# Performance work log

Measured on AMD Instinct MI355X. Metric: run time of the kernel, lower is better.

Reference implementation:

```python
import jax, jax.numpy as jnp
import numpy as np

B, N, D_FEAT = 16, 1024, 64
NPOINT, RADIUS, NSAMPLE = 512, 0.2, 32
EPS = 1e-5


def _square_distance(src, dst):
    # src [b,S,3], dst [b,N,3] -> [b,S,N]
    d = -2.0 * jnp.einsum('bsc,bnc->bsn', src, dst)
    d = d + jnp.sum(src * src, -1)[:, :, None]
    d = d + jnp.sum(dst * dst, -1)[:, None, :]
    return d


def _fps(xyz, npoint):
    # xyz [b,N,3] -> indices [b,npoint]; seeded by point farthest from the mean
    b, n, _ = xyz.shape
    centroid = jnp.mean(xyz, axis=1, keepdims=True)
    distance = jnp.minimum(jnp.full((b, n), 1e10, xyz.dtype),
                           jnp.sum((xyz - centroid) ** 2, -1))
    farthest = jnp.argmax(distance, -1)
    bidx = jnp.arange(b)

    def body(carry, _):
        dist, far = carry
        c = xyz[bidx[:, None], far[:, None]]  # [b,1,3]
        dist = jnp.minimum(dist, jnp.sum((xyz - c) ** 2, -1))
        return (dist, jnp.argmax(dist, -1)), far

    _, idx = jax.lax.scan(body, (distance, farthest), None, length=npoint)
    return idx.T  # [b, npoint]


def _gather(points, idx):
    # points [b,N,C], idx [b,...] -> [b,...,C]
    return jax.vmap(lambda p, i: p[i])(points, idx)


def _query_ball(radius, nsample, xyz, new_xyz):
    # faithful to torch: mask out-of-radius with N, full sort, take first nsample,
    # replace sentinels by the first (closest-index) in-ball point
    b, n, _ = xyz.shape
    sqr = _square_distance(new_xyz, xyz)  # [b,S,N]
    idx = jnp.where(sqr > radius ** 2, n, jnp.arange(n)[None, None, :])
    idx = jnp.sort(idx, axis=-1)[:, :, :nsample]
    first = idx[:, :, :1]
    return jnp.where(idx == n, first, idx)


def _qbn(x):
    # QBN_RM training mode: divide by per-channel RMS of detached activations
    mean = jnp.mean(jax.lax.stop_gradient(x) ** 2, axis=(0, 2, 3))
    return x / jnp.sqrt(mean + EPS)[None, :, None, None]


def _qrelu(x):
    # scale each 3-vector by mod / max(mod, 1), coefficient detached
    b3, c, s, k = x.shape
    b = b3 // 3
    xd = jax.lax.stop_gradient(x).reshape(b, 3, c, s, k)
    mod = jnp.sqrt(jnp.sum(xd * xd, axis=1))  # [b,c,s,k]
    coeff = mod / jnp.maximum(mod, 1.0)
    return jnp.broadcast_to(coeff[:, None], (b, 3, c, s, k)).reshape(b3, c, s, k) * x


def _qmaxpool(x):
    # our_mpool1d with kernel (1, nsample): pick the max-modulus sample over K,
    # gather the same index for all 3 quaternion components
    b3, c, s, k = x.shape
    b = b3 // 3
    x5 = x.reshape(b, 3, c, s, k)
    mod = jnp.sum(jax.lax.stop_gradient(x5) ** 2, axis=1)  # argmax of mod == argmax of mod^2
    idx = jnp.argmax(mod, axis=-1)  # [b,c,s]
    idxb = jnp.broadcast_to(idx[:, None, :, :, None], (b, 3, c, s, 1))
    y = jnp.take_along_axis(x5, idxb, axis=-1)[..., 0]  # [b,3,c,s]
    return y.reshape(b3, c, s)


def setup_inputs() -> dict:
    key = jax.random.key(0)
    k1, k2, k3, k4, k5 = jax.random.split(key, 5)
    xyz = jax.random.normal(k1, (B, 3, N), dtype=jnp.float32)
    points = jax.random.normal(k2, (B * 3, D_FEAT, N), dtype=jnp.float32)
    W0 = jax.random.normal(k3, (64, 66), dtype=jnp.float32) * np.sqrt(2.0 / 66)
    W1 = jax.random.normal(k4, (64, 64), dtype=jnp.float32) * np.sqrt(2.0 / 64)
    W2 = jax.random.normal(k5, (128, 64), dtype=jnp.float32) * np.sqrt(2.0 / 64)
    return {"xyz": xyz, "points": points, "W0": W0, "W1": W1, "W2": W2}


def reference(xyz, points, W0, W1, W2):
    xyz_t = xyz.transpose(0, 2, 1)      # [B,N,3]
    pts_t = points.transpose(0, 2, 1)   # [B*3,N,D]

    fps_idx = _fps(xyz_t, NPOINT)                       # [B,S]
    new_xyz = _gather(xyz_t, fps_idx)                   # [B,S,3]
    idx = _query_ball(RADIUS, NSAMPLE, xyz_t, new_xyz)  # [B,S,K]

    g_xyz = _gather(xyz_t, idx)                         # [B,S,K,3]
    g_norm = g_xyz - new_xyz[:, :, None, :]
    gx = g_xyz.transpose(0, 3, 1, 2).reshape(B * 3, NPOINT, NSAMPLE, 1)
    gn = g_norm.transpose(0, 3, 1, 2).reshape(B * 3, NPOINT, NSAMPLE, 1)
    idx3 = jnp.broadcast_to(idx[:, None], (B, 3, NPOINT, NSAMPLE)).reshape(B * 3, NPOINT, NSAMPLE)
    gp = _gather(pts_t, idx3)                           # [B*3,S,K,D]

    x = jnp.concatenate([gn, gx, gp], axis=-1)          # [B*3,S,K,D+2]
    x = x.transpose(0, 3, 1, 2)                         # [B*3,D+2,S,K]
    for W in (W0, W1, W2):
        x = jnp.einsum('bcsk,oc->bosk', x, W)           # 1x1 conv, no bias
        x = _qrelu(_qbn(x))
    new_feat = _qmaxpool(x)                             # [B*3,128,S]
    return new_xyz.transpose(0, 2, 1), new_feat
```

## Files before the change

kernel.cpp:

```cpp
#include <hip/hip_runtime.h>

typedef unsigned int u32;

#define NB 16
#define NPT 1024
#define NP 512
#define NS 32
#define DF 64
#define RAD2 0.04f
#define EPSQ 1e-5f
#define CNTF 786432.0f
#define NGRP 8192
#define TCAP 96
#define TSLOT 128
#define NTILE_MAX 2731

__device__ __forceinline__ float rmul(float a, float b){ return __fmul_rn(a,b); }
__device__ __forceinline__ float radd(float a, float b){ return __fadd_rn(a,b); }
__device__ __forceinline__ float sq3(float a, float b, float c){
  return radd(radd(rmul(a,a), rmul(b,b)), rmul(c,c));
}

__device__ __forceinline__ float wave_sum64(float v){
  #pragma unroll
  for(int m=1;m<64;m<<=1) v += __shfl_xor(v, m, 64);
  return v;
}

template<int PT>
__global__ __launch_bounds__(256) void fps_combo(const float* __restrict__ xyz,
                                                 float* __restrict__ out0,
                                                 const float* __restrict__ pts,
                                                 float* __restrict__ ptsT,
                                                 u32* __restrict__ witem){
  const int bid = blockIdx.x;
  const int t = threadIdx.x;
  if(bid >= NB){
    const int gid = (bid - NB)*256 + t;
    if(gid < NTILE_MAX*TSLOT) witem[gid] = 0xFFFFFFFFu;
    if constexpr(PT){
      const int w = gid >> 6, ln = gid & 63;
      if(w < 48*16){
        const int b3 = w >> 4, n0 = (w & 15) << 6;
        const float* src = pts + (((size_t)b3*64 + ln) << 10);
        float* dst = ptsT + (((size_t)b3*1024 + n0) << 6) + ln;
        #pragma unroll 4
        for(int i=0;i<64;i++) dst[(size_t)i << 6] = src[n0 + i];
      }
    }
    return;
  }
  if(t >= 64) return;
  const int lane = t;
  const int b = bid;
  const float* xb = xyz + b*3*NPT;
  float px[16], py[16], pz[16], dist[16];
  #pragma unroll
  for(int j=0;j<16;j++){
    const int n = lane*16 + j;
    px[j] = xb[n]; py[j] = xb[NPT+n]; pz[j] = xb[2*NPT+n];
  }
  float sx=0.f, sy=0.f, sz=0.f;
  #pragma unroll
  for(int j=0;j<16;j++){ sx+=px[j]; sy+=py[j]; sz+=pz[j]; }
  sx = wave_sum64(sx); sy = wave_sum64(sy); sz = wave_sum64(sz);
  const float cx = sx/1024.f, cy = sy/1024.f, cz = sz/1024.f;
  float m = -1.f; int mi = 0;
  #pragma unroll
  for(int j=0;j<16;j++){
    float dx = px[j]-cx, dy = py[j]-cy, dz = pz[j]-cz;
    float d = fminf(1e10f, sq3(dx,dy,dz));
    dist[j] = d;
    if(d > m){ m = d; mi = lane*16 + j; }
  }
  #pragma unroll
  for(int msk=1; msk<64; msk<<=1){
    float ov = __shfl_xor(m, msk, 64); int oi = __shfl_xor(mi, msk, 64);
    if(ov > m || (ov == m && oi < mi)){ m = ov; mi = oi; }
  }
  int far = mi;
  for(int it=0; it<NP; ++it){
    const float qx = xb[far], qy = xb[NPT+far], qz = xb[2*NPT+far];
    if(lane == 0){
      out0[(b*3+0)*NP + it] = qx;
      out0[(b*3+1)*NP + it] = qy;
      out0[(b*3+2)*NP + it] = qz;
    }
    m = -1.f; mi = 0;
    #pragma unroll
    for(int j=0;j<16;j++){
      float dx = px[j]-qx, dy = py[j]-qy, dz = pz[j]-qz;
      float nd = sq3(dx,dy,dz);
      float d = fminf(dist[j], nd);
      dist[j] = d;
      if(d > m){ m = d; mi = lane*16 + j; }
    }
    #pragma unroll
    for(int msk=1; msk<64; msk<<=1){
      float ov = __shfl_xor(m, msk, 64); int oi = __shfl_xor(mi, msk, 64);
      if(ov > m || (ov == m && oi < mi)){ m = ov; mi = oi; }
    }
    far = mi;
  }
}

__global__ __launch_bounds__(256) void ball_kernel(const float* __restrict__ xyz,
                                                   const float* __restrict__ out0,
                                                   int* __restrict__ idxb,
                                                   int* __restrict__ cntb){
  const int gw = (blockIdx.x * 256 + threadIdx.x) >> 6;
  const int lane = threadIdx.x & 63;
  const int b = gw >> 9;
  const int s = gw & 511;
  const float s0 = out0[(b*3+0)*NP + s];
  const float s1 = out0[(b*3+1)*NP + s];
  const float s2 = out0[(b*3+2)*NP + s];
  const float ss = sq3(s0,s1,s2);
  const float* xb = xyz + b*3*NPT;
  int base = 0;
  int* row = idxb + (b*NP + s)*NS;
  for(int chk=0; chk<16 && base<NS; ++chk){
    const int n = chk*64 + lane;
    float d0 = xb[n], d1 = xb[NPT+n], d2 = xb[2*NPT+n];
    float dd = sq3(d0,d1,d2);
    float p  = radd(radd(rmul(s0,d0), rmul(s1,d1)), rmul(s2,d2));
    float sqr = radd(radd(rmul(-2.0f,p), ss), dd);
    bool inc = !(sqr > RAD2);
    unsigned long long mask = __ballot(inc);
    if(inc){
      int slot = base + __popcll(mask & ((1ull<<lane)-1ull));
      if(slot < NS) row[slot] = n;
    }
    base += __popcll(mask);
  }
  if(lane==0) cntb[gw] = (base < NS) ? base : NS;
}

__global__ __launch_bounds__(256) void pack_kernel(const int* __restrict__ cntb,
                                                   const int* __restrict__ idxb,
                                                   u32* __restrict__ witem,
                                                   int* __restrict__ ntile_dev){
  __shared__ int tsum[256];
  const int t = threadIdx.x;
  int s0 = 0;
  #pragma unroll 4
  for(int i=0;i<32;i++) s0 += cntb[t*32+i];
  tsum[t] = s0;
  __syncthreads();
  for(int ofs=1; ofs<256; ofs<<=1){
    int v = (t >= ofs) ? tsum[t-ofs] : 0;
    __syncthreads();
    tsum[t] += v;
    __syncthreads();
  }
  int m = tsum[t] - s0;
  if(t==255) *ntile_dev = (tsum[255] + TCAP - 1) / TCAP;
  for(int i=0;i<32;i++){
    int g = t*32+i; int c = cntb[g];
    int tile = m / TCAP; int slot = m - TCAP*tile;
    const int* row = idxb + g*NS;
    for(int j=0;j<c;j++){
      witem[tile*TSLOT + slot + j] = (u32)((g<<15) | (j<<10) | row[j]);
    }
    m += c;
  }
}

template<int DEPTH, int PT>
__global__ __launch_bounds__(384) void pass_kernel(
  const float* __restrict__ xyz, const float* __restrict__ ptsrc,
  const float* __restrict__ W0, const float* __restrict__ W1, const float* __restrict__ W2,
  const float* __restrict__ out0, const u32* __restrict__ witem,
  const int* __restrict__ cntb, const int* __restrict__ ntile_dev,
  const float* __restrict__ inv1, const float* __restrict__ inv2,
  float* __restrict__ part, float* __restrict__ out1)
{
  const int t = threadIdx.x;
  const int c3 = t >> 7;
  const int r  = t & 127;
  const int lane = t & 63;
  const int wv = t >> 6;
  const int bi = blockIdx.x;
  constexpr int nch = (DEPTH==3) ? 128 : 64;

  if(bi >= *ntile_dev){
    if(t < nch) part[bi*nch + t] = 0.f;
    return;
  }

  __shared__ float sq[3][128][17];
  __shared__ float wstat[6][128];
  for(int i=t; i<6*128; i+=384) (&wstat[0][0])[i] = 0.f;
  __syncthreads();

  const u32 w = witem[bi*TSLOT + r];
  const bool valid = (w != 0xFFFFFFFFu);
  const int bs = valid ? (int)(w >> 15) : 0;
  const int j  = valid ? (int)((w >> 10) & 31) : 1;
  const int n  = valid ? (int)(w & 1023) : 0;
  const int b = bs >> 9;
  const int s = bs & 511;
  const int b3 = b*3 + c3;
  const int cv = cntb[bs];
  const float wgt = valid ? ((j==0) ? (float)(33 - cv) : 1.0f) : 0.0f;

  const float gx = xyz[b3*NPT + n];
  const float cx = out0[b3*NP + s];
  float x0[66];
  x0[0] = gx - cx;
  x0[1] = gx;
  if constexpr(PT){
    const float4* pr4 = reinterpret_cast<const float4*>(ptsrc + (((size_t)b3<<10) + (size_t)n)*DF);
    #pragma unroll
    for(int q=0;q<16;q++){
      float4 v = pr4[q];
      x0[2+4*q] = v.x; x0[3+4*q] = v.y; x0[4+4*q] = v.z; x0[5+4*q] = v.w;
    }
  } else {
    const float* pr = ptsrc + ((size_t)b3*DF)*NPT + n;
    #pragma unroll
    for(int c=0;c<DF;c++) x0[2+c] = pr[(size_t)c*NPT];
  }

  float y1[64];
  #pragma unroll
  for(int ch=0; ch<4; ++ch){
    float acc[16];
    #pragma unroll
    for(int oo=0;oo<16;oo++){
      const int o = ch*16+oo;
      float a = 0.f;
      #pragma unroll
      for(int c=0;c<66;c++) a = fmaf(W0[o*66+c], x0[c], a);
      acc[oo] = a;
    }
    if constexpr(DEPTH == 1){
      #pragma unroll
      for(int oo=0;oo<16;oo++){
        float v = wave_sum64(acc[oo]*acc[oo]*wgt);
        if(lane==0) wstat[wv][ch*16+oo] += v;
      }
    } else {
      #pragma unroll
      for(int oo=0;oo<16;oo++){
        const int o = ch*16+oo;
        float xp = acc[oo] * inv1[o];
        acc[oo] = xp;
        sq[c3][r][oo] = xp*xp;
      }
      __syncthreads();
      #pragma unroll
      for(int oo=0;oo<16;oo++){
        float m2 = (sq[0][r][oo] + sq[1][r][oo]) + sq[2][r][oo];
        float mod = sqrtf(m2);
        float cf = (mod >= 1.f) ? 1.f : mod;
        y1[ch*16+oo] = cf * acc[oo];
      }
      __syncthreads();
    }
  }
  if constexpr(DEPTH == 1){
    __syncthreads();
    if(t < 64){
      float sv = 0.f;
      #pragma unroll
      for(int wq=0;wq<6;wq++) sv += wstat[wq][t];
      part[bi*64 + t] = sv;
    }
    return;
  }

  float y2[64];
  #pragma unroll
  for(int ch=0; ch<4; ++ch){
    float acc[16];
    #pragma unroll
    for(int oo=0;oo<16;oo++){
      const int o = ch*16+oo;
      float a = 0.f;
      #pragma unroll
      for(int c=0;c<64;c++) a = fmaf(W1[o*64+c], y1[c], a);
      acc[oo] = a;
    }
    if constexpr(DEPTH == 2){
      #pragma unroll
      for(int oo=0;oo<16;oo++){
        float v = wave_sum64(acc[oo]*acc[oo]*wgt);
        if(lane==0) wstat[wv][ch*16+oo] += v;
      }
    } else {
      #pragma unroll
      for(int oo=0;oo<16;oo++){
        const int o = ch*16+oo;
        float xp = acc[oo] * inv2[o];
        acc[oo] = xp;
        sq[c3][r][oo] = xp*xp;
      }
      __syncthreads();
      #pragma unroll
      for(int oo=0;oo<16;oo++){
        float m2 = (sq[0][r][oo] + sq[1][r][oo]) + sq[2][r][oo];
        float mod = sqrtf(m2);
        float cf = (mod >= 1.f) ? 1.f : mod;
        y2[ch*16+oo] = cf * acc[oo];
      }
      __syncthreads();
    }
  }
  if constexpr(DEPTH == 2){
    __syncthreads();
    if(t < 64){
      float sv = 0.f;
      #pragma unroll
      for(int wq=0;wq<6;wq++) sv += wstat[wq][t];
      part[bi*64 + t] = sv;
    }
    return;
  }

  #pragma unroll
  for(int ch=0; ch<8; ++ch){
    float a3[16];
    #pragma unroll
    for(int oo=0;oo<16;oo++){
      const int o = ch*16+oo;
      float a = 0.f;
      #pragma unroll
      for(int c=0;c<64;c++) a = fmaf(W2[o*64+c], y2[c], a);
      a3[oo] = a;
      sq[c3][r][oo] = a;
    }
    __syncthreads();
    if(c3 == 0){
      #pragma unroll
      for(int oo=0;oo<16;oo++){
        float a0 = sq[0][r][oo], a1 = sq[1][r][oo], a2 = sq[2][r][oo];
        float m2 = radd(radd(rmul(a0,a0), rmul(a1,a1)), rmul(a2,a2));
        float v = wave_sum64(m2*wgt);
        if(lane==0) wstat[wv][ch*16+oo] += v;
        if(valid && j==0){
          float bvv = m2; int bjj = 0;
          for(int jj=1; jj<cv; ++jj){
            float c0 = sq[0][r+jj][oo], c1 = sq[1][r+jj][oo], c2 = sq[2][r+jj][oo];
            float mm = radd(radd(rmul(c0,c0), rmul(c1,c1)), rmul(c2,c2));
            if(mm > bvv){ bvv = mm; bjj = jj; }
          }
          const int o = ch*16+oo;
          #pragma unroll
          for(int cc=0;cc<3;cc++){
            out1[(((size_t)(3*b+cc))*128 + o)*NP + s] = sq[cc][r+bjj][oo];
          }
        }
      }
    }
    __syncthreads();
  }
  if(t < 128){
    part[bi*128 + t] = wstat[0][t] + wstat[1][t];
  }
}

__global__ __launch_bounds__(256) void fin_kernel(const float* __restrict__ part, int nblk, int nch,
                                                  float* __restrict__ inv){
  const int o = blockIdx.x;
  const int t = threadIdx.x;
  float sum = 0.f;
  for(int i=t; i<nblk; i+=256) sum += part[(size_t)i*nch + o];
  sum = wave_sum64(sum);
  __shared__ float red[4];
  if((t&63)==0) red[t>>6] = sum;
  __syncthreads();
  if(t==0){
    float tot = (red[0]+red[1])+(red[2]+red[3]);
    inv[o] = 1.0f / sqrtf(tot/CNTF + EPSQ);
  }
}

__global__ __launch_bounds__(256) void scale_kernel(float* __restrict__ out,
                                                    const float* __restrict__ inv3){
  const int tid = blockIdx.x*256 + threadIdx.x;
  if(tid >= NB*128*NP) return;
  const int s = tid & 511;
  const int o = (tid >> 9) & 127;
  const int b = tid >> 16;
  float* base = out + NB*3*NP;
  const size_t str = (size_t)128*NP;
  size_t i0 = ((size_t)(b*3)*128 + o)*NP + s;
  float iv = inv3[o];
  float a0 = base[i0] * iv;
  float a1 = base[i0+str] * iv;
  float a2 = base[i0+2*str] * iv;
  float m2 = (a0*a0 + a1*a1) + a2*a2;
  float mod = sqrtf(m2);
  float cf = (mod >= 1.f) ? 1.f : mod;
  base[i0] = cf*a0; base[i0+str] = cf*a1; base[i0+2*str] = cf*a2;
}

extern "C" void kernel_launch(void* const* d_in, const int* in_sizes, int n_in,
                              void* d_out, int out_size, void* d_ws, size_t ws_size,
                              hipStream_t stream){
  const float* xyz = (const float*)d_in[0];
  const float* pts = (const float*)d_in[1];
  const float* W0  = (const float*)d_in[2];
  const float* W1  = (const float*)d_in[3];
  const float* W2  = (const float*)d_in[4];
  float* out = (float*)d_out;

  char* p = (char*)d_ws;
  auto carve = [&](size_t bytes)->char*{
    char* q = p; p += (bytes + 255) & ~(size_t)255; return q;
  };
  int*   idxb      = (int*)  carve((size_t)NGRP*NS*4);
  int*   cntb      = (int*)  carve((size_t)NGRP*4);
  u32*   witem     = (u32*)  carve((size_t)NTILE_MAX*TSLOT*4);
  int*   ntile_dev = (int*)  carve(256);
  float* part1     = (float*)carve((size_t)NTILE_MAX*64*4);
  float* part2     = (float*)carve((size_t)NTILE_MAX*64*4);
  float* part3     = (float*)carve((size_t)NTILE_MAX*128*4);
  float* inv1      = (float*)carve(64*4);
  float* inv2      = (float*)carve(64*4);
  float* inv3      = (float*)carve(128*4);
  size_t base_need = (size_t)(p - (char*)d_ws);
  float* ptsT      = (float*)p;
  const size_t pt_bytes = (size_t)48*1024*64*4;
  const bool use_pt = (ws_size >= base_need + pt_bytes);

  float* out1 = out + NB*3*NP;

  const int copyblk = (NTILE_MAX*TSLOT + 255)/256;
  if(use_pt) fps_combo<1><<<NB + copyblk, 256, 0, stream>>>(xyz, out, pts, ptsT, witem);
  else       fps_combo<0><<<NB + copyblk, 256, 0, stream>>>(xyz, out, pts, nullptr, witem);

  ball_kernel<<<2048, 256, 0, stream>>>(xyz, out, idxb, cntb);
  pack_kernel<<<1, 256, 0, stream>>>(cntb, idxb, witem, ntile_dev);

  if(use_pt){
    pass_kernel<1,1><<<NTILE_MAX, 384, 0, stream>>>(xyz, ptsT, W0, W1, W2, out, witem, cntb, ntile_dev, nullptr, nullptr, part1, nullptr);
    fin_kernel<<<64, 256, 0, stream>>>(part1, NTILE_MAX, 64, inv1);
    pass_kernel<2,1><<<NTILE_MAX, 384, 0, stream>>>(xyz, ptsT, W0, W1, W2, out, witem, cntb, ntile_dev, inv1, nullptr, part2, nullptr);
    fin_kernel<<<64, 256, 0, stream>>>(part2, NTILE_MAX, 64, inv2);
    pass_kernel<3,1><<<NTILE_MAX, 384, 0, stream>>>(xyz, ptsT, W0, W1, W2, out, witem, cntb, ntile_dev, inv1, inv2, part3, out1);
  } else {
    pass_kernel<1,0><<<NTILE_MAX, 384, 0, stream>>>(xyz, pts, W0, W1, W2, out, witem, cntb, ntile_dev, nullptr, nullptr, part1, nullptr);
    fin_kernel<<<64, 256, 0, stream>>>(part1, NTILE_MAX, 64, inv1);
    pass_kernel<2,0><<<NTILE_MAX, 384, 0, stream>>>(xyz, pts, W0, W1, W2, out, witem, cntb, ntile_dev, inv1, nullptr, part2, nullptr);
    fin_kernel<<<64, 256, 0, stream>>>(part2, NTILE_MAX, 64, inv2);
    pass_kernel<3,0><<<NTILE_MAX, 384, 0, stream>>>(xyz, pts, W0, W1, W2, out, witem, cntb, ntile_dev, inv1, inv2, part3, out1);
  }
  fin_kernel<<<128, 256, 0, stream>>>(part3, NTILE_MAX, 128, inv3);
  scale_kernel<<<(NB*128*NP + 255)/256, 256, 0, stream>>>(out, inv3);
}
```

Before: 925.7 us.

## Use DPP tree argmax in FPS, parallel scan pack, fuse final stats with scale

```diff
diff --git a/kernel.cpp b/kernel.cpp
--- a/kernel.cpp
+++ b/kernel.cpp
@@ -25,6 +25,44 @@
   #pragma unroll
   for(int m=1;m<64;m<<=1) v += __shfl_xor(v, m, 64);
   return v;
+}
+
+#define DPPCOMB(CTRL) do{ \
+  float _ov = __int_as_float(__builtin_amdgcn_mov_dpp(__float_as_int(m), (CTRL), 0xF, 0xF, true)); \
+  int   _oi = __builtin_amdgcn_mov_dpp(mi, (CTRL), 0xF, 0xF, true); \
+  if(_ov > m || (_ov == m && _oi < mi)){ m = _ov; mi = _oi; } \
+}while(0)
+
+__device__ __forceinline__ int wave_argmax1024(const float* dist, int lane){
+  float v8[8]; int j8[8];
+  #pragma unroll
+  for(int q=0;q<8;q++){
+    float l = dist[q], r = dist[q+8];
+    bool tk = (r > l);
+    v8[q] = tk ? r : l; j8[q] = tk ? q+8 : q;
+  }
+  float v4[4]; int j4[4];
+  #pragma unroll
+  for(int q=0;q<4;q++){
+    bool tk = (v8[q+4] > v8[q]);
+    v4[q] = tk ? v8[q+4] : v8[q]; j4[q] = tk ? j8[q+4] : j8[q];
+  }
+  float v2[2]; int j2[2];
+  #pragma unroll
+  for(int q=0;q<2;q++){
+    bool tk = (v4[q+2] > v4[q]);
+    v2[q] = tk ? v4[q+2] : v4[q]; j2[q] = tk ? j4[q+2] : j4[q];
+  }
+  bool tk = (v2[1] > v2[0]);
+  float m = tk ? v2[1] : v2[0];
+  int mi = lane*16 + (tk ? j2[1] : j2[0]);
+  DPPCOMB(0xB1);
+  DPPCOMB(0x4E);
+  DPPCOMB(0x124);
+  DPPCOMB(0x128);
+  DPPCOMB(0x142);
+  DPPCOMB(0x143);
+  return __builtin_amdgcn_readlane(mi, 63);
 }
 
 template<int PT>
@@ -65,20 +103,12 @@
   for(int j=0;j<16;j++){ sx+=px[j]; sy+=py[j]; sz+=pz[j]; }
   sx = wave_sum64(sx); sy = wave_sum64(sy); sz = wave_sum64(sz);
   const float cx = sx/1024.f, cy = sy/1024.f, cz = sz/1024.f;
-  float m = -1.f; int mi = 0;
   #pragma unroll
   for(int j=0;j<16;j++){
     float dx = px[j]-cx, dy = py[j]-cy, dz = pz[j]-cz;
-    float d = fminf(1e10f, sq3(dx,dy,dz));
-    dist[j] = d;
-    if(d > m){ m = d; mi = lane*16 + j; }
-  }
-  #pragma unroll
-  for(int msk=1; msk<64; msk<<=1){
-    float ov = __shfl_xor(m, msk, 64); int oi = __shfl_xor(mi, msk, 64);
-    if(ov > m || (ov == m && oi < mi)){ m = ov; mi = oi; }
-  }
-  int far = mi;
+    dist[j] = fminf(1e10f, sq3(dx,dy,dz));
+  }
+  int far = wave_argmax1024(dist, lane);
   for(int it=0; it<NP; ++it){
     const float qx = xb[far], qy = xb[NPT+far], qz = xb[2*NPT+far];
     if(lane == 0){
@@ -86,21 +116,13 @@
       out0[(b*3+1)*NP + it] = qy;
       out0[(b*3+2)*NP + it] = qz;
     }
-    m = -1.f; mi = 0;
     #pragma unroll
     for(int j=0;j<16;j++){
       float dx = px[j]-qx, dy = py[j]-qy, dz = pz[j]-qz;
       float nd = sq3(dx,dy,dz);
-      float d = fminf(dist[j], nd);
-      dist[j] = d;
-      if(d > m){ m = d; mi = lane*16 + j; }
-    }
-    #pragma unroll
-    for(int msk=1; msk<64; msk<<=1){
-      float ov = __shfl_xor(m, msk, 64); int oi = __shfl_xor(mi, msk, 64);
-      if(ov > m || (ov == m && oi < mi)){ m = ov; mi = oi; }
-    }
-    far = mi;
+      dist[j] = fminf(dist[j], nd);
+    }
+    far = wave_argmax1024(dist, lane);
   }
 }
 
@@ -136,33 +158,39 @@
   if(lane==0) cntb[gw] = (base < NS) ? base : NS;
 }
 
-__global__ __launch_bounds__(256) void pack_kernel(const int* __restrict__ cntb,
-                                                   const int* __restrict__ idxb,
-                                                   u32* __restrict__ witem,
-                                                   int* __restrict__ ntile_dev){
-  __shared__ int tsum[256];
+__global__ __launch_bounds__(1024) void pack_kernel(const int* __restrict__ cntb,
+                                                    const int* __restrict__ idxb,
+                                                    u32* __restrict__ witem,
+                                                    int* __restrict__ ntile_dev){
   const int t = threadIdx.x;
-  int s0 = 0;
-  #pragma unroll 4
-  for(int i=0;i<32;i++) s0 += cntb[t*32+i];
-  tsum[t] = s0;
+  const int lane = t & 63;
+  const int wv = t >> 6;
+  int c[8]; int s0 = 0;
+  #pragma unroll
+  for(int i=0;i<8;i++){ c[i] = cntb[t*8+i]; s0 += c[i]; }
+  int pre = s0;
+  #pragma unroll
+  for(int d=1; d<64; d<<=1){
+    int v = __shfl_up(pre, d, 64);
+    if(lane >= d) pre += v;
+  }
+  __shared__ int wsum[16];
+  if(lane==63) wsum[wv] = pre;
   __syncthreads();
-  for(int ofs=1; ofs<256; ofs<<=1){
-    int v = (t >= ofs) ? tsum[t-ofs] : 0;
-    __syncthreads();
-    tsum[t] += v;
-    __syncthreads();
-  }
-  int m = tsum[t] - s0;
-  if(t==255) *ntile_dev = (tsum[255] + TCAP - 1) / TCAP;
-  for(int i=0;i<32;i++){
-    int g = t*32+i; int c = cntb[g];
-    int tile = m / TCAP; int slot = m - TCAP*tile;
+  int wo = 0;
+  #pragma unroll
+  for(int w=0;w<16;w++) if(w < wv) wo += wsum[w];
+  int m = wo + pre - s0;
+  if(t==1023) *ntile_dev = (wo + pre + TCAP - 1) / TCAP;
+  #pragma unroll
+  for(int i=0;i<8;i++){
+    const int g = t*8+i; const int cc = c[i];
+    const int tile = m / TCAP; const int slot = m - TCAP*tile;
     const int* row = idxb + g*NS;
-    for(int j=0;j<c;j++){
+    for(int j=0;j<cc;j++){
       witem[tile*TSLOT + slot + j] = (u32)((g<<15) | (j<<10) | row[j]);
     }
-    m += c;
+    m += cc;
   }
 }
 
@@ -181,12 +209,8 @@
   const int lane = t & 63;
   const int wv = t >> 6;
   const int bi = blockIdx.x;
-  constexpr int nch = (DEPTH==3) ? 128 : 64;
-
-  if(bi >= *ntile_dev){
-    if(t < nch) part[bi*nch + t] = 0.f;
-    return;
-  }
+
+  if(bi >= *ntile_dev) return;
 
   __shared__ float sq[3][128][17];
   __shared__ float wstat[6][128];
@@ -360,10 +384,12 @@
   }
 }
 
-__global__ __launch_bounds__(256) void fin_kernel(const float* __restrict__ part, int nblk, int nch,
+__global__ __launch_bounds__(256) void fin_kernel(const float* __restrict__ part,
+                                                  const int* __restrict__ ntile_dev, int nch,
                                                   float* __restrict__ inv){
   const int o = blockIdx.x;
   const int t = threadIdx.x;
+  const int nblk = *ntile_dev;
   float sum = 0.f;
   for(int i=t; i<nblk; i+=256) sum += part[(size_t)i*nch + o];
   sum = wave_sum64(sum);
@@ -376,24 +402,38 @@
   }
 }
 
-__global__ __launch_bounds__(256) void scale_kernel(float* __restrict__ out,
-                                                    const float* __restrict__ inv3){
-  const int tid = blockIdx.x*256 + threadIdx.x;
-  if(tid >= NB*128*NP) return;
-  const int s = tid & 511;
-  const int o = (tid >> 9) & 127;
-  const int b = tid >> 16;
+__global__ __launch_bounds__(256) void fin3_scale(const float* __restrict__ part3,
+                                                  const int* __restrict__ ntile_dev,
+                                                  float* __restrict__ out){
+  const int o = blockIdx.x;
+  const int t = threadIdx.x;
+  const int nblk = *ntile_dev;
+  float sum = 0.f;
+  for(int i=t; i<nblk; i+=256) sum += part3[(size_t)i*128 + o];
+  sum = wave_sum64(sum);
+  __shared__ float red[4];
+  __shared__ float sinv;
+  if((t&63)==0) red[t>>6] = sum;
+  __syncthreads();
+  if(t==0){
+    float tot = (red[0]+red[1])+(red[2]+red[3]);
+    sinv = 1.0f / sqrtf(tot/CNTF + EPSQ);
+  }
+  __syncthreads();
+  const float iv = sinv;
   float* base = out + NB*3*NP;
   const size_t str = (size_t)128*NP;
-  size_t i0 = ((size_t)(b*3)*128 + o)*NP + s;
-  float iv = inv3[o];
-  float a0 = base[i0] * iv;
-  float a1 = base[i0+str] * iv;
-  float a2 = base[i0+2*str] * iv;
-  float m2 = (a0*a0 + a1*a1) + a2*a2;
-  float mod = sqrtf(m2);
-  float cf = (mod >= 1.f) ? 1.f : mod;
-  base[i0] = cf*a0; base[i0+str] = cf*a1; base[i0+2*str] = cf*a2;
+  for(int idx=t; idx<NB*NP; idx+=256){
+    const int b = idx >> 9, s = idx & 511;
+    size_t i0 = ((size_t)(b*3)*128 + o)*NP + s;
+    float a0 = base[i0] * iv;
+    float a1 = base[i0+str] * iv;
+    float a2 = base[i0+2*str] * iv;
+    float m2 = (a0*a0 + a1*a1) + a2*a2;
+    float mod = sqrtf(m2);
+    float cf = (mod >= 1.f) ? 1.f : mod;
+    base[i0] = cf*a0; base[i0+str] = cf*a1; base[i0+2*str] = cf*a2;
+  }
 }
 
 extern "C" void kernel_launch(void* const* d_in, const int* in_sizes, int n_in,
@@ -432,21 +472,20 @@
   else       fps_combo<0><<<NB + copyblk, 256, 0, stream>>>(xyz, out, pts, nullptr, witem);
 
   ball_kernel<<<2048, 256, 0, stream>>>(xyz, out, idxb, cntb);
-  pack_kernel<<<1, 256, 0, stream>>>(cntb, idxb, witem, ntile_dev);
+  pack_kernel<<<1, 1024, 0, stream>>>(cntb, idxb, witem, ntile_dev);
 
   if(use_pt){
     pass_kernel<1,1><<<NTILE_MAX, 384, 0, stream>>>(xyz, ptsT, W0, W1, W2, out, witem, cntb, ntile_dev, nullptr, nullptr, part1, nullptr);
-    fin_kernel<<<64, 256, 0, stream>>>(part1, NTILE_MAX, 64, inv1);
+    fin_kernel<<<64, 256, 0, stream>>>(part1, ntile_dev, 64, inv1);
     pass_kernel<2,1><<<NTILE_MAX, 384, 0, stream>>>(xyz, ptsT, W0, W1, W2, out, witem, cntb, ntile_dev, inv1, nullptr, part2, nullptr);
-    fin_kernel<<<64, 256, 0, stream>>>(part2, NTILE_MAX, 64, inv2);
+    fin_kernel<<<64, 256, 0, stream>>>(part2, ntile_dev, 64, inv2);
     pass_kernel<3,1><<<NTILE_MAX, 384, 0, stream>>>(xyz, ptsT, W0, W1, W2, out, witem, cntb, ntile_dev, inv1, inv2, part3, out1);
   } else {
     pass_kernel<1,0><<<NTILE_MAX, 384, 0, stream>>>(xyz, pts, W0, W1, W2, out, witem, cntb, ntile_dev, nullptr, nullptr, part1, nullptr);
-    fin_kernel<<<64, 256, 0, stream>>>(part1, NTILE_MAX, 64, inv1);
+    fin_kernel<<<64, 256, 0, stream>>>(part1, ntile_dev, 64, inv1);
     pass_kernel<2,0><<<NTILE_MAX, 384, 0, stream>>>(xyz, pts, W0, W1, W2, out, witem, cntb, ntile_dev, inv1, nullptr, part2, nullptr);
-    fin_kernel<<<64, 256, 0, stream>>>(part2, NTILE_MAX, 64, inv2);
+    fin_kernel<<<64, 256, 0, stream>>>(part2, ntile_dev, 64, inv2);
     pass_kernel<3,0><<<NTILE_MAX, 384, 0, stream>>>(xyz, pts, W0, W1, W2, out, witem, cntb, ntile_dev, inv1, inv2, part3, out1);
   }
-  fin_kernel<<<128, 256, 0, stream>>>(part3, NTILE_MAX, 128, inv3);
-  scale_kernel<<<(NB*128*NP + 255)/256, 256, 0, stream>>>(out, inv3);
-}
+  fin3_scale<<<128, 256, 0, stream>>>(part3, ntile_dev, out);
+}
```

Result: faster. 830.6 us (-10.3%).
